# Performance work log

Hardware: AMD Instinct MI355X
Metric: run time of the kernel (lower is better)

Reference implementation:

```python
import jax, jax.numpy as jnp
import numpy as np

NT, NS, NF, NG, NH, ND, HS = 365, 128, 6, 16, 8, 366, 256
EPS = 1e-6


def _divide_p(p, t1, t2):
    # func.divideP: rain/snow partition via arccos temperature interpolation
    r = jnp.clip((t1 + t2) / jnp.maximum(t2 - t1, EPS), -1.0, 1.0)
    vf = jnp.arccos(r) / jnp.pi
    vf = jnp.where(t1 >= 0, 0.0, vf)
    vf = jnp.where(t2 <= 0, 1.0, vf)
    return p * vf, p * (1.0 - vf)  # Ps (snow), Pl (liquid)


def _hard_sigmoid(x):
    return jnp.clip(x / 6.0 + 0.5, 0.0, 1.0)


def setup_inputs():
    key = jax.random.key(0)
    ks = jax.random.split(key, 11)
    prcp = jax.random.uniform(ks[0], (NT, NS)) * 10.0
    evp = jax.random.uniform(ks[1], (NT, NS)) * 5.0
    t1 = jax.random.normal(ks[2], (NT, NS)) * 10.0
    t2 = t1 + jax.random.uniform(ks[3], (NT, NS)) * 10.0 + 0.1
    rad = jax.random.normal(ks[4], (NT, NS))
    hum = jax.random.normal(ks[5], (NT, NS))
    x = jnp.stack([prcp, evp, t1, t2, rad, hum], axis=-1)  # (NT, NS, 6)
    xc = jax.random.normal(ks[6], (NS, NG))

    def lin(k, fan_out, fan_in):
        b = 1.0 / np.sqrt(fan_in)
        kw, kb = jax.random.split(k)
        return (jax.random.uniform(kw, (fan_out, fan_in), minval=-b, maxval=b),
                jax.random.uniform(kb, (fan_out,), minval=-b, maxval=b))

    W_fc, b_fc = lin(ks[7], HS, NG)
    W_g, b_g = lin(ks[8], NH * 6, HS)
    W_kin, b_kin = lin(ks[9], HS, 4)
    W_kout, b_kout = lin(ks[10], NH * 1, HS)
    return dict(x=x, xc=xc, W_fc=W_fc, b_fc=b_fc, W_g=W_g, b_g=b_g,
                W_kin=W_kin, b_kin=b_kin, W_kout=W_kout, b_kout=b_kout)


def reference(x, xc, W_fc, b_fc, W_g, b_g, W_kin, b_kin, W_kout, b_kout):
    prcp, evp, t1, t2 = x[..., 0], x[..., 1], x[..., 2], x[..., 3]
    ps, pl = _divide_p(prcp, t1, t2)  # (NT, NS)
    f = x[..., 2:]  # (NT, NS, 4) time-varying features T1,T2,Rad,Hum

    # getParam (eval mode -> DropMask is identity)
    state = xc @ W_fc.T + b_fc                                   # (NS, HS)
    pk = jnp.tanh(f @ W_kin.T + b_kin + state) @ W_kout.T + b_kout  # (NT, NS, NH)
    pg = jnp.tanh(state) @ W_g.T + b_g                           # (NS, 6*NH)
    km = jnp.exp(pk)                                             # melt rate
    gk = jnp.exp(pg[:, 0:NH]) / 100.0                            # recession
    gl = jnp.exp(pg[:, NH:2 * NH]) * 100.0                       # capacity
    qb = jax.nn.relu(pg[:, 2 * NH:3 * NH]) / 10.0                # baseflow
    ga = jax.nn.softmax(pg[:, 3 * NH:4 * NH], axis=-1)           # bucket areas
    gi = _hard_sigmoid(pg[:, 4 * NH:5 * NH]) / 2.0               # infiltration frac
    ge = jax.nn.relu(pg[:, 5 * NH:6 * NH])                       # evap factor

    sf0 = jnp.zeros((NS, NH), x.dtype)
    d0 = jnp.zeros((NS, NH, ND), x.dtype)

    @jax.checkpoint
    def step(carry, inp):
        sf, d = carry
        ps_t, pl_t, ev_t, km_t = inp
        # snow bucket
        sf1 = sf + ps_t[:, None]
        melt = jnp.minimum(sf1, km_t)
        sf_new = sf1 - melt
        w_in = melt + pl_t[:, None] * gi           # inflow to soil (NS, NH)
        e_pot = ev_t[:, None] * ge
        # StorAge-Selection: age-rank shift, oldest bin pools
        d_sh = jnp.concatenate([w_in[..., None], d[..., :-1]], axis=-1)
        d_sh = d_sh.at[..., -1].add(d[..., -1])
        s = d_sh.sum(-1)
        # evaporation, uniform over ages, capped by storage
        f_ev = jnp.clip(e_pot / jnp.maximum(s, EPS), 0.0, 1.0)
        d1 = d_sh * (1.0 - f_ev[..., None])
        s1 = s * (1.0 - f_ev)
        # surface spill above capacity gl
        q_s = jax.nn.relu(s1 - gl)
        f_s = q_s / jnp.maximum(s1, EPS)
        d2 = d1 * (1.0 - f_s[..., None])
        s2 = s1 - q_s
        # uniform-SAS subsurface discharge
        q_sub = jnp.minimum(s2 * gk + qb, s2)
        f_q = q_sub / jnp.maximum(s2, EPS)
        q_age = d2 * f_q[..., None]                # flux[1]: per-age outflow
        q_age = q_age.at[..., 0].add(q_s)
        d_new = d2 * (1.0 - f_q[..., None])
        q = jnp.sum(q_age.sum(-1) * ga, axis=-1)   # area-weighted discharge (NS,)
        return (sf_new, d_new), q

    (_, _), q_pred = jax.lax.scan(step, (sf0, d0), (ps, pl, evp, km))
    return q_pred  # (NT, NS)
```

## Files before the change

kernel.cpp:

```cpp
#include <hip/hip_runtime.h>
#include <math.h>

#define NT 365
#define NT2 368
#define NS 128
#define NG 16
#define NH 8
#define HS 256
#define NSNH (NS * NH)
#define EPSC 1e-6f

#define WS_PRM 0
#define WS_P   8192

__device__ __forceinline__ float fast_rcp(float v) {
#if __has_builtin(__builtin_amdgcn_rcpf)
    return __builtin_amdgcn_rcpf(v);
#else
    return 1.f / v;
#endif
}
__device__ __forceinline__ float fast_tanh(float xv) {
    float e = __expf(2.f * xv);
    return 1.f - 2.f * fast_rcp(e + 1.f);
}

__global__ __launch_bounds__(256) void k_main(
    const float* __restrict__ x, const float* __restrict__ xc,
    const float* __restrict__ W_fc, const float* __restrict__ b_fc,
    const float* __restrict__ W_g, const float* __restrict__ b_g,
    const float* __restrict__ W_kin, const float* __restrict__ b_kin,
    const float* __restrict__ W_kout, const float* __restrict__ b_kout,
    float* __restrict__ prm, float4* __restrict__ P)
{
    __shared__ float us[HS];
    __shared__ float ts[HS];
    __shared__ __align__(16) float4 wkin_lds[HS];
    __shared__ float wko_lds[8 * 260];
    __shared__ __align__(16) float lds_u[4 * 288];
    __shared__ float pgs[6 * NH];

    int tid = threadIdx.x;
    int wave = tid >> 6, lane = tid & 63;
    int s = blockIdx.x & 127;
    int t0 = (blockIdx.x >> 7) * 4 + wave;
    int h = lane >> 3, jg = lane & 7;

    wkin_lds[tid] = ((const float4*)W_kin)[tid];
#pragma unroll
    for (int i = 0; i < 8; ++i) {
        int idx = tid + 256 * i;
        wko_lds[(idx >> 8) * 260 + (idx & 255)] = W_kout[idx];
    }
    {
        float a = b_fc[tid];
        const float4* wf = (const float4*)(W_fc + tid * NG);
        const float* xr = xc + s * NG;
#pragma unroll
        for (int i = 0; i < 4; ++i) {
            float4 w = wf[i];
            a += xr[4*i] * w.x + xr[4*i+1] * w.y + xr[4*i+2] * w.z + xr[4*i+3] * w.w;
        }
        ts[tid] = tanhf(a);
        us[tid] = a + b_kin[tid];
    }
    __syncthreads();

    float ust[4]; float4 w4[4];
#pragma unroll
    for (int r = 0; r < 4; ++r) {
        ust[r] = us[lane + 64 * r];
        w4[r]  = wkin_lds[lane + 64 * r];
    }
    float4 wwr[8];
#pragma unroll
    for (int k = 0; k < 8; ++k)
        wwr[k] = *(const float4*)(wko_lds + h * 260 + jg * 32 + 4 * k);
    float bko = b_kout[h];

    if (blockIdx.x < NS) {
        for (int k = wave; k < 6 * NH; k += 4) {
            float p = 0.f;
#pragma unroll
            for (int r = 0; r < 4; ++r) {
                int jj = lane + 64 * r;
                p += ts[jj] * W_g[k * HS + jj];
            }
#pragma unroll
            for (int off = 32; off; off >>= 1) p += __shfl_xor(p, off, 64);
            if (lane == 0) pgs[k] = p + b_g[k];
        }
        __syncthreads();
        if (tid < NH) {
            int hh = tid;
            float gk = expf(pgs[hh]) * 0.01f;
            float gl = expf(pgs[NH + hh]) * 100.f;
            float qb = fmaxf(pgs[2 * NH + hh], 0.f) * 0.1f;
            float m = pgs[3 * NH];
#pragma unroll
            for (int i = 1; i < NH; ++i) m = fmaxf(m, pgs[3 * NH + i]);
            float den = 0.f;
#pragma unroll
            for (int i = 0; i < NH; ++i) den += expf(pgs[3 * NH + i] - m);
            float ga = expf(pgs[3 * NH + hh] - m) / den;
            float gi = fminf(fmaxf(pgs[4 * NH + hh] * (1.f / 6.f) + 0.5f, 0.f), 1.f) * 0.5f;
            float ge = fmaxf(pgs[5 * NH + hh], 0.f);
            int o = s * NH + hh;
            prm[0 * NSNH + o] = gk;
            prm[1 * NSNH + o] = gl;
            prm[2 * NSNH + o] = qb;
            prm[3 * NSNH + o] = ga;
            prm[4 * NSNH + o] = gi;
            prm[5 * NSNH + o] = ge;
        }
    }

    float* uw = lds_u + wave * 288;
    int ubase = lane + 4 * (lane >> 5);
    const float4* uuP = (const float4*)(uw + jg * 36);
    int sblk = s >> 3, srem = (s & 7) * 8;

#pragma unroll
    for (int g = 0; g < 8; ++g) {
        int t = t0 + 48 * g;
        if (t >= NT) {
            if (t < NT2 && jg == 0)
                P[(sblk * NT2 + t) * 64 + srem + h] = make_float4(0.f, 0.f, 0.f, 0.f);
            continue;
        }
        const float2* xr2 = (const float2*)(x + (size_t)(t * NS + s) * 6);
        float2 a01 = xr2[0], a23 = xr2[1], a45 = xr2[2];
        float prcp = a01.x, ev = a01.y;
        float f0 = a23.x, f1 = a23.y, f2 = a45.x, f3 = a45.y;
#pragma unroll
        for (int r = 0; r < 4; ++r) {
            float uval = fast_tanh(ust[r] + f0 * w4[r].x + f1 * w4[r].y +
                                   f2 * w4[r].z + f3 * w4[r].w);
            uw[ubase + 72 * r] = uval;
        }
        float r_ = (f0 + f1) / fmaxf(f1 - f0, EPSC);
        r_ = fminf(fmaxf(r_, -1.f), 1.f);
        float vf = acosf(r_) * 0.31830988618379067f;
        if (f0 >= 0.f) vf = 0.f;
        if (f1 <= 0.f) vf = 1.f;
        float psv = prcp * vf;
        float plv = prcp * (1.f - vf);
        float acc = 0.f;
#pragma unroll
        for (int k = 0; k < 8; ++k) {
            float4 a = uuP[k], b = wwr[k];
            acc += a.x * b.x + a.y * b.y + a.z * b.z + a.w * b.w;
        }
        acc += __shfl_xor(acc, 1, 64);
        acc += __shfl_xor(acc, 2, 64);
        acc += __shfl_xor(acc, 4, 64);
        if (jg == 0)
            P[(sblk * NT2 + t) * 64 + srem + h] =
                make_float4(__expf(acc + bko), psv, plv, ev);
    }
}

__global__ __launch_bounds__(64, 1) void k_scan(
    const float4* __restrict__ P, const float* __restrict__ prm,
    float* __restrict__ q)
{
    int lane = threadIdx.x;
    int blk = blockIdx.x;
    int sbase = blk * 8;
    int gofs = blk * 64 + lane;

    float gk = prm[0 * NSNH + gofs];
    float gl = prm[1 * NSNH + gofs];
    float qb = prm[2 * NSNH + gofs];
    float gi = prm[4 * NSNH + gofs];
    float ge = prm[5 * NSNH + gofs];
    float c1 = 1.f - gk, nqb = -qb, nge = -ge;
    int ss0 = lane & 7;
    float gar[8];
#pragma unroll
    for (int hh = 0; hh < 8; ++hh)
        gar[hh] = prm[3 * NSNH + (sbase + ss0) * 8 + hh];

    __shared__ float out_lds[64 * 17];
    float S = 0.f, sf = 0.f;
    const float4* Pb = P + (size_t)blk * (NT2 * 64) + lane;

    float4 A[16], B[16], C[16];

#define LOADC(ci, BUF) { const float4* p_ = Pb + (ci) * 1024; _Pragma("unroll") \
    for (int c = 0; c < 16; ++c) BUF[c] = p_[c * 64]; }

#define WORKC(BUF, tb) { \
    _Pragma("unroll") for (int c = 0; c < 16; ++c) { \
        float4 a = BUF[c]; \
        float sf1 = sf + a.y; \
        float melt = fminf(sf1, a.x); \
        sf = sf1 - melt; \
        float Sw = S + fmaf(a.z, gi, melt); \
        float t2v = fmaf(a.w, nge, Sw); \
        float S1 = fmaxf(t2v, 0.f); \
        float S2 = __builtin_amdgcn_fmed3f(t2v, 0.f, gl); \
        float Sn = fmaxf(fmaf(S2, c1, nqb), 0.f); \
        S = Sn; \
        out_lds[lane * 17 + c] = S1 - Sn; \
    } \
    _Pragma("unroll") for (int it = 0; it < 2; ++it) { \
        int idx = it * 64 + lane; int c = idx >> 3; \
        float sum = 0.f; \
        _Pragma("unroll") for (int hh = 0; hh < 8; ++hh) \
            sum = fmaf(gar[hh], out_lds[(ss0 * 8 + hh) * 17 + c], sum); \
        int t = (tb) + c; \
        if (t < NT) q[t * NS + sbase + ss0] = sum; \
    } }

    LOADC(0, A); LOADC(1, B);
    for (int k = 0; k < 7; ++k) {
        int c3 = 3 * k;
        LOADC(c3 + 2, C); WORKC(A, c3 * 16);
        LOADC(c3 + 3, A); WORKC(B, (c3 + 1) * 16);
        LOADC(c3 + 4, B); WORKC(C, (c3 + 2) * 16);
    }
    WORKC(A, 21 * 16); WORKC(B, 22 * 16);
#undef LOADC
#undef WORKC
}

extern "C" void kernel_launch(void* const* d_in, const int* in_sizes, int n_in,
                              void* d_out, int out_size, void* d_ws, size_t ws_size,
                              hipStream_t stream)
{
    const float* x      = (const float*)d_in[0];
    const float* xc     = (const float*)d_in[1];
    const float* W_fc   = (const float*)d_in[2];
    const float* b_fc   = (const float*)d_in[3];
    const float* W_g    = (const float*)d_in[4];
    const float* b_g    = (const float*)d_in[5];
    const float* W_kin  = (const float*)d_in[6];
    const float* b_kin  = (const float*)d_in[7];
    const float* W_kout = (const float*)d_in[8];
    const float* b_kout = (const float*)d_in[9];
    float* q = (float*)d_out;

    float* ws  = (float*)d_ws;
    float* prm = ws + WS_PRM;
    float4* P  = (float4*)(ws + WS_P);

    hipLaunchKernelGGL(k_main, dim3(1536), dim3(256), 0, stream,
                       x, xc, W_fc, b_fc, W_g, b_g, W_kin, b_kin,
                       W_kout, b_kout, prm, P);

    hipLaunchKernelGGL(k_scan, dim3(16), dim3(64), 0, stream,
                       P, prm, q);
}
```

Baseline: 38.13 us.

## Compute per-timestep kinetic MLP in one thread over hidden dim, shrink grid

Replaces the wave-cooperative layout (lanes split across hidden units, LDS exchange and shuffle reductions) with one thread per timestep looping over all 256 hidden units. It accumulates the 8 outputs in registers using broadcast LDS reads of transposed W_kout. The grid shrinks from 1536 to 256 blocks, and each block covers 184 timesteps for one site. This removes the shuffles and redundant prologue work per block, but gives each thread a long serial loop and leaves fewer threads active, with 72 of 256 idle per block.

```diff
diff --git a/kernel.cpp b/kernel.cpp
--- a/kernel.cpp
+++ b/kernel.cpp
@@ -20,10 +20,14 @@
     return 1.f / v;
 #endif
 }
-__device__ __forceinline__ float fast_tanh(float xv) {
-    float e = __expf(2.f * xv);
-    return 1.f - 2.f * fast_rcp(e + 1.f);
-}
+__device__ __forceinline__ float fexp2(float v) {
+#if __has_builtin(__builtin_amdgcn_exp2f)
+    return __builtin_amdgcn_exp2f(v);
+#else
+    return exp2f(v);
+#endif
+}
+#define TWO_LOG2E 2.8853900817779268f
 
 __global__ __launch_bounds__(256) void k_main(
     const float* __restrict__ x, const float* __restrict__ xc,
@@ -33,24 +37,25 @@
     const float* __restrict__ W_kout, const float* __restrict__ b_kout,
     float* __restrict__ prm, float4* __restrict__ P)
 {
-    __shared__ float us[HS];
+    __shared__ float u0[HS];
     __shared__ float ts[HS];
     __shared__ __align__(16) float4 wkin_lds[HS];
-    __shared__ float wko_lds[8 * 260];
-    __shared__ __align__(16) float lds_u[4 * 288];
+    __shared__ __align__(16) float4 wkoA[HS];
+    __shared__ __align__(16) float4 wkoB[HS];
     __shared__ float pgs[6 * NH];
 
     int tid = threadIdx.x;
-    int wave = tid >> 6, lane = tid & 63;
     int s = blockIdx.x & 127;
-    int t0 = (blockIdx.x >> 7) * 4 + wave;
-    int h = lane >> 3, jg = lane & 7;
+    int th = blockIdx.x >> 7;
 
     wkin_lds[tid] = ((const float4*)W_kin)[tid];
-#pragma unroll
-    for (int i = 0; i < 8; ++i) {
-        int idx = tid + 256 * i;
-        wko_lds[(idx >> 8) * 260 + (idx & 255)] = W_kout[idx];
+    {
+        float4 va, vb;
+        va.x = W_kout[0 * HS + tid]; va.y = W_kout[1 * HS + tid];
+        va.z = W_kout[2 * HS + tid]; va.w = W_kout[3 * HS + tid];
+        vb.x = W_kout[4 * HS + tid]; vb.y = W_kout[5 * HS + tid];
+        vb.z = W_kout[6 * HS + tid]; vb.w = W_kout[7 * HS + tid];
+        wkoA[tid] = va; wkoB[tid] = vb;
     }
     {
         float a = b_fc[tid];
@@ -62,23 +67,12 @@
             a += xr[4*i] * w.x + xr[4*i+1] * w.y + xr[4*i+2] * w.z + xr[4*i+3] * w.w;
         }
         ts[tid] = tanhf(a);
-        us[tid] = a + b_kin[tid];
+        u0[tid] = a + b_kin[tid];
     }
     __syncthreads();
 
-    float ust[4]; float4 w4[4];
-#pragma unroll
-    for (int r = 0; r < 4; ++r) {
-        ust[r] = us[lane + 64 * r];
-        w4[r]  = wkin_lds[lane + 64 * r];
-    }
-    float4 wwr[8];
-#pragma unroll
-    for (int k = 0; k < 8; ++k)
-        wwr[k] = *(const float4*)(wko_lds + h * 260 + jg * 32 + 4 * k);
-    float bko = b_kout[h];
-
     if (blockIdx.x < NS) {
+        int wave = tid >> 6, lane = tid & 63;
         for (int k = wave; k < 6 * NH; k += 4) {
             float p = 0.f;
 #pragma unroll
@@ -115,49 +109,55 @@
         }
     }
 
-    float* uw = lds_u + wave * 288;
-    int ubase = lane + 4 * (lane >> 5);
-    const float4* uuP = (const float4*)(uw + jg * 36);
-    int sblk = s >> 3, srem = (s & 7) * 8;
-
-#pragma unroll
-    for (int g = 0; g < 8; ++g) {
-        int t = t0 + 48 * g;
-        if (t >= NT) {
-            if (t < NT2 && jg == 0)
-                P[(sblk * NT2 + t) * 64 + srem + h] = make_float4(0.f, 0.f, 0.f, 0.f);
-            continue;
-        }
-        const float2* xr2 = (const float2*)(x + (size_t)(t * NS + s) * 6);
-        float2 a01 = xr2[0], a23 = xr2[1], a45 = xr2[2];
-        float prcp = a01.x, ev = a01.y;
-        float f0 = a23.x, f1 = a23.y, f2 = a45.x, f3 = a45.y;
-#pragma unroll
-        for (int r = 0; r < 4; ++r) {
-            float uval = fast_tanh(ust[r] + f0 * w4[r].x + f1 * w4[r].y +
-                                   f2 * w4[r].z + f3 * w4[r].w);
-            uw[ubase + 72 * r] = uval;
-        }
-        float r_ = (f0 + f1) / fmaxf(f1 - f0, EPSC);
-        r_ = fminf(fmaxf(r_, -1.f), 1.f);
-        float vf = acosf(r_) * 0.31830988618379067f;
-        if (f0 >= 0.f) vf = 0.f;
-        if (f1 <= 0.f) vf = 1.f;
-        float psv = prcp * vf;
-        float plv = prcp * (1.f - vf);
-        float acc = 0.f;
-#pragma unroll
-        for (int k = 0; k < 8; ++k) {
-            float4 a = uuP[k], b = wwr[k];
-            acc += a.x * b.x + a.y * b.y + a.z * b.z + a.w * b.w;
-        }
-        acc += __shfl_xor(acc, 1, 64);
-        acc += __shfl_xor(acc, 2, 64);
-        acc += __shfl_xor(acc, 4, 64);
-        if (jg == 0)
-            P[(sblk * NT2 + t) * 64 + srem + h] =
-                make_float4(__expf(acc + bko), psv, plv, ev);
-    }
+    if (tid >= 184) return;
+    int t = th * 184 + tid;
+    float4* Pb = P + ((size_t)(s >> 3) * NT2 + t) * 64 + (s & 7) * 8;
+
+    if (t >= NT) {
+        float4 z = make_float4(0.f, 0.f, 0.f, 0.f);
+#pragma unroll
+        for (int h = 0; h < NH; ++h) Pb[h] = z;
+        return;
+    }
+
+    const float* xr = x + (size_t)(t * NS + s) * 6;
+    float prcp = xr[0], ev = xr[1], f0 = xr[2], f1 = xr[3], f2 = xr[4], f3 = xr[5];
+
+    float a0 = 0.f, a1 = 0.f, a2 = 0.f, a3 = 0.f;
+    float a4 = 0.f, a5 = 0.f, a6 = 0.f, a7 = 0.f;
+#pragma unroll 4
+    for (int j = 0; j < HS; ++j) {
+        float4 w = wkin_lds[j];
+        float arg = u0[j];
+        arg = fmaf(f0, w.x, arg);
+        arg = fmaf(f1, w.y, arg);
+        arg = fmaf(f2, w.z, arg);
+        arg = fmaf(f3, w.w, arg);
+        float e = fexp2(arg * TWO_LOG2E);
+        float tn = 1.f - 2.f * fast_rcp(e + 1.f);
+        float4 wa = wkoA[j], wb = wkoB[j];
+        a0 = fmaf(tn, wa.x, a0); a1 = fmaf(tn, wa.y, a1);
+        a2 = fmaf(tn, wa.z, a2); a3 = fmaf(tn, wa.w, a3);
+        a4 = fmaf(tn, wb.x, a4); a5 = fmaf(tn, wb.y, a5);
+        a6 = fmaf(tn, wb.z, a6); a7 = fmaf(tn, wb.w, a7);
+    }
+
+    float r_ = (f0 + f1) / fmaxf(f1 - f0, EPSC);
+    r_ = fminf(fmaxf(r_, -1.f), 1.f);
+    float vf = acosf(r_) * 0.31830988618379067f;
+    if (f0 >= 0.f) vf = 0.f;
+    if (f1 <= 0.f) vf = 1.f;
+    float psv = prcp * vf;
+    float plv = prcp * (1.f - vf);
+
+    Pb[0] = make_float4(__expf(a0 + b_kout[0]), psv, plv, ev);
+    Pb[1] = make_float4(__expf(a1 + b_kout[1]), psv, plv, ev);
+    Pb[2] = make_float4(__expf(a2 + b_kout[2]), psv, plv, ev);
+    Pb[3] = make_float4(__expf(a3 + b_kout[3]), psv, plv, ev);
+    Pb[4] = make_float4(__expf(a4 + b_kout[4]), psv, plv, ev);
+    Pb[5] = make_float4(__expf(a5 + b_kout[5]), psv, plv, ev);
+    Pb[6] = make_float4(__expf(a6 + b_kout[6]), psv, plv, ev);
+    Pb[7] = make_float4(__expf(a7 + b_kout[7]), psv, plv, ev);
 }
 
 __global__ __launch_bounds__(64, 1) void k_scan(
@@ -245,7 +245,7 @@
     float* prm = ws + WS_PRM;
     float4* P  = (float4*)(ws + WS_P);
 
-    hipLaunchKernelGGL(k_main, dim3(1536), dim3(256), 0, stream,
+    hipLaunchKernelGGL(k_main, dim3(256), dim3(256), 0, stream,
                        x, xc, W_fc, b_fc, W_g, b_g, W_kin, b_kin,
                        W_kout, b_kout, prm, P);
 
```

After: 43.37 us. 1.14x slower.

## Warp-specialize scan: producer waves stage P via LDS ring, consumer reduces outputs

Applied to the files above, without the earlier changes.

The scan kernel becomes four waves. One wave runs the serial recurrence while three waves prefetch input chunks into a triple-buffered LDS ring and do the area-weighted output reduction from a double-buffered LDS output buffer. The main kernel now folds the gi and ge coefficients into a single precomputed inflow term, so the serial chain does fewer FMAs per step. To do that, every k_main block computes the parameter projection, not only the first 128. The change aims to take load latency and reduction work off the serial critical path, at the cost of a block-wide barrier per chunk and redundant parameter work in k_main.

```diff
diff --git a/kernel.cpp b/kernel.cpp
--- a/kernel.cpp
+++ b/kernel.cpp
@@ -9,6 +9,8 @@
 #define HS 256
 #define NSNH (NS * NH)
 #define EPSC 1e-6f
+#define CH 16
+#define NCH 23
 
 #define WS_PRM 0
 #define WS_P   8192
@@ -19,10 +21,6 @@
 #else
     return 1.f / v;
 #endif
-}
-__device__ __forceinline__ float fast_tanh(float xv) {
-    float e = __expf(2.f * xv);
-    return 1.f - 2.f * fast_rcp(e + 1.f);
 }
 
 __global__ __launch_bounds__(256) void k_main(
@@ -39,6 +37,7 @@
     __shared__ float wko_lds[8 * 260];
     __shared__ __align__(16) float lds_u[4 * 288];
     __shared__ float pgs[6 * NH];
+    __shared__ float gie[NH], gee[NH];
 
     int tid = threadIdx.x;
     int wave = tid >> 6, lane = tid & 63;
@@ -78,42 +77,48 @@
         wwr[k] = *(const float4*)(wko_lds + h * 260 + jg * 32 + 4 * k);
     float bko = b_kout[h];
 
-    if (blockIdx.x < NS) {
-        for (int k = wave; k < 6 * NH; k += 4) {
-            float p = 0.f;
-#pragma unroll
-            for (int r = 0; r < 4; ++r) {
-                int jj = lane + 64 * r;
-                p += ts[jj] * W_g[k * HS + jj];
-            }
-#pragma unroll
-            for (int off = 32; off; off >>= 1) p += __shfl_xor(p, off, 64);
-            if (lane == 0) pgs[k] = p + b_g[k];
-        }
-        __syncthreads();
-        if (tid < NH) {
-            int hh = tid;
-            float gk = expf(pgs[hh]) * 0.01f;
-            float gl = expf(pgs[NH + hh]) * 100.f;
-            float qb = fmaxf(pgs[2 * NH + hh], 0.f) * 0.1f;
-            float m = pgs[3 * NH];
-#pragma unroll
-            for (int i = 1; i < NH; ++i) m = fmaxf(m, pgs[3 * NH + i]);
-            float den = 0.f;
-#pragma unroll
-            for (int i = 0; i < NH; ++i) den += expf(pgs[3 * NH + i] - m);
-            float ga = expf(pgs[3 * NH + hh] - m) / den;
-            float gi = fminf(fmaxf(pgs[4 * NH + hh] * (1.f / 6.f) + 0.5f, 0.f), 1.f) * 0.5f;
-            float ge = fmaxf(pgs[5 * NH + hh], 0.f);
-            int o = s * NH + hh;
-            prm[0 * NSNH + o] = gk;
-            prm[1 * NSNH + o] = gl;
-            prm[2 * NSNH + o] = qb;
-            prm[3 * NSNH + o] = ga;
-            prm[4 * NSNH + o] = gi;
-            prm[5 * NSNH + o] = ge;
-        }
-    }
+    for (int k = wave; k < 6 * NH; k += 4) {
+        float p = 0.f;
+#pragma unroll
+        for (int r = 0; r < 4; ++r) {
+            int jj = lane + 64 * r;
+            p += ts[jj] * W_g[k * HS + jj];
+        }
+#pragma unroll
+        for (int off = 32; off; off >>= 1) p += __shfl_xor(p, off, 64);
+        if (lane == 0) pgs[k] = p + b_g[k];
+    }
+    __syncthreads();
+
+    if (tid < NH) {
+        gie[tid] = fminf(fmaxf(pgs[4 * NH + tid] * (1.f / 6.f) + 0.5f, 0.f), 1.f) * 0.5f;
+        gee[tid] = fmaxf(pgs[5 * NH + tid], 0.f);
+    }
+    if (blockIdx.x < NS && tid < NH) {
+        int hh = tid;
+        float gk = expf(pgs[hh]) * 0.01f;
+        float gl = expf(pgs[NH + hh]) * 100.f;
+        float qb = fmaxf(pgs[2 * NH + hh], 0.f) * 0.1f;
+        float m = pgs[3 * NH];
+#pragma unroll
+        for (int i = 1; i < NH; ++i) m = fmaxf(m, pgs[3 * NH + i]);
+        float den = 0.f;
+#pragma unroll
+        for (int i = 0; i < NH; ++i) den += expf(pgs[3 * NH + i] - m);
+        float ga = expf(pgs[3 * NH + hh] - m) / den;
+        float gi = fminf(fmaxf(pgs[4 * NH + hh] * (1.f / 6.f) + 0.5f, 0.f), 1.f) * 0.5f;
+        float ge = fmaxf(pgs[5 * NH + hh], 0.f);
+        int o = s * NH + hh;
+        prm[0 * NSNH + o] = gk;
+        prm[1 * NSNH + o] = gl;
+        prm[2 * NSNH + o] = qb;
+        prm[3 * NSNH + o] = ga;
+        prm[4 * NSNH + o] = gi;
+        prm[5 * NSNH + o] = ge;
+    }
+    __syncthreads();
+
+    float gih = gie[h], geh = gee[h];
 
     float* uw = lds_u + wave * 288;
     int ubase = lane + 4 * (lane >> 5);
@@ -134,9 +139,9 @@
         float f0 = a23.x, f1 = a23.y, f2 = a45.x, f3 = a45.y;
 #pragma unroll
         for (int r = 0; r < 4; ++r) {
-            float uval = fast_tanh(ust[r] + f0 * w4[r].x + f1 * w4[r].y +
-                                   f2 * w4[r].z + f3 * w4[r].w);
-            uw[ubase + 72 * r] = uval;
+            float e = __expf(2.f * (ust[r] + f0 * w4[r].x + f1 * w4[r].y +
+                                    f2 * w4[r].z + f3 * w4[r].w));
+            uw[ubase + 72 * r] = 1.f - 2.f * fast_rcp(e + 1.f);
         }
         float r_ = (f0 + f1) / fmaxf(f1 - f0, EPSC);
         r_ = fminf(fmaxf(r_, -1.f), 1.f);
@@ -156,73 +161,112 @@
         acc += __shfl_xor(acc, 4, 64);
         if (jg == 0)
             P[(sblk * NT2 + t) * 64 + srem + h] =
-                make_float4(__expf(acc + bko), psv, plv, ev);
-    }
-}
-
-__global__ __launch_bounds__(64, 1) void k_scan(
+                make_float4(__expf(acc + bko), psv, plv * gih - ev * geh, 0.f);
+    }
+}
+
+__global__ __launch_bounds__(256, 1) void k_scan(
     const float4* __restrict__ P, const float* __restrict__ prm,
     float* __restrict__ q)
 {
-    int lane = threadIdx.x;
+    __shared__ __align__(16) float4 ring[3][CH][64];
+    __shared__ float outb[2][CH * 72];
+
+    int tid = threadIdx.x, wave = tid >> 6, lane = tid & 63;
     int blk = blockIdx.x;
-    int sbase = blk * 8;
-    int gofs = blk * 64 + lane;
-
-    float gk = prm[0 * NSNH + gofs];
-    float gl = prm[1 * NSNH + gofs];
-    float qb = prm[2 * NSNH + gofs];
-    float gi = prm[4 * NSNH + gofs];
-    float ge = prm[5 * NSNH + gofs];
-    float c1 = 1.f - gk, nqb = -qb, nge = -ge;
-    int ss0 = lane & 7;
+    const float4* Pb = P + (size_t)blk * (NT2 * 64);
+
+    if (wave == 0) {
+        int gofs = blk * 64 + lane;
+        float gk = prm[0 * NSNH + gofs];
+        float gl = prm[1 * NSNH + gofs];
+        float qb = prm[2 * NSNH + gofs];
+        float c1 = 1.f - gk, nqb = -qb;
+        float S = 0.f, sf = 0.f;
+        int obase = (lane >> 3) * 9 + (lane & 7);
+        __syncthreads();
+        for (int c = 0; c < NCH; ++c) {
+            const float4* rs = &ring[c % 3][0][lane];
+            float* ob = &outb[c & 1][obase];
+#pragma unroll
+            for (int st = 0; st < CH; ++st) {
+                float4 a = rs[st * 64];
+                float sf1 = sf + a.y;
+                float melt = fminf(sf1, a.x);
+                sf = sf1 - melt;
+                float t2v = (S + a.z) + melt;
+                float S1 = fmaxf(t2v, 0.f);
+                float S2 = __builtin_amdgcn_fmed3f(t2v, 0.f, gl);
+                float Sn = fmaxf(fmaf(S2, c1, nqb), 0.f);
+                S = Sn;
+                ob[st * 72] = S1 - Sn;
+            }
+            __syncthreads();
+        }
+        return;
+    }
+
+    int w = wave - 1;
+    int nrows = (w == 0) ? 6 : 5;
+    float4 regs[6];
+    int sq = lane & 7;
     float gar[8];
-#pragma unroll
-    for (int hh = 0; hh < 8; ++hh)
-        gar[hh] = prm[3 * NSNH + (sbase + ss0) * 8 + hh];
-
-    __shared__ float out_lds[64 * 17];
-    float S = 0.f, sf = 0.f;
-    const float4* Pb = P + (size_t)blk * (NT2 * 64) + lane;
-
-    float4 A[16], B[16], C[16];
-
-#define LOADC(ci, BUF) { const float4* p_ = Pb + (ci) * 1024; _Pragma("unroll") \
-    for (int c = 0; c < 16; ++c) BUF[c] = p_[c * 64]; }
-
-#define WORKC(BUF, tb) { \
-    _Pragma("unroll") for (int c = 0; c < 16; ++c) { \
-        float4 a = BUF[c]; \
-        float sf1 = sf + a.y; \
-        float melt = fminf(sf1, a.x); \
-        sf = sf1 - melt; \
-        float Sw = S + fmaf(a.z, gi, melt); \
-        float t2v = fmaf(a.w, nge, Sw); \
-        float S1 = fmaxf(t2v, 0.f); \
-        float S2 = __builtin_amdgcn_fmed3f(t2v, 0.f, gl); \
-        float Sn = fmaxf(fmaf(S2, c1, nqb), 0.f); \
-        S = Sn; \
-        out_lds[lane * 17 + c] = S1 - Sn; \
-    } \
-    _Pragma("unroll") for (int it = 0; it < 2; ++it) { \
-        int idx = it * 64 + lane; int c = idx >> 3; \
-        float sum = 0.f; \
-        _Pragma("unroll") for (int hh = 0; hh < 8; ++hh) \
-            sum = fmaf(gar[hh], out_lds[(ss0 * 8 + hh) * 17 + c], sum); \
-        int t = (tb) + c; \
-        if (t < NT) q[t * NS + sbase + ss0] = sum; \
-    } }
-
-    LOADC(0, A); LOADC(1, B);
-    for (int k = 0; k < 7; ++k) {
-        int c3 = 3 * k;
-        LOADC(c3 + 2, C); WORKC(A, c3 * 16);
-        LOADC(c3 + 3, A); WORKC(B, (c3 + 1) * 16);
-        LOADC(c3 + 4, B); WORKC(C, (c3 + 2) * 16);
-    }
-    WORKC(A, 21 * 16); WORKC(B, 22 * 16);
-#undef LOADC
-#undef WORKC
+    if (w >= 1) {
+#pragma unroll
+        for (int hh = 0; hh < 8; ++hh)
+            gar[hh] = prm[3 * NSNH + (blk * 8 + sq) * 8 + hh];
+    }
+#pragma unroll
+    for (int ck = 0; ck < 2; ++ck) {
+        for (int i = 0; i < 6; ++i) {
+            int row = w + 3 * i;
+            if (i < nrows) regs[i] = Pb[(ck * CH + row) * 64 + lane];
+        }
+        for (int i = 0; i < 6; ++i) {
+            int row = w + 3 * i;
+            if (i < nrows) ring[ck][row][lane] = regs[i];
+        }
+    }
+    for (int i = 0; i < 6; ++i) {
+        int row = w + 3 * i;
+        if (i < nrows) regs[i] = Pb[(2 * CH + row) * 64 + lane];
+    }
+    __syncthreads();
+
+    for (int c = 0; c < NCH; ++c) {
+        if (c + 2 < NCH) {
+            int slot = (c + 2) % 3;
+            for (int i = 0; i < 6; ++i) {
+                int row = w + 3 * i;
+                if (i < nrows) ring[slot][row][lane] = regs[i];
+            }
+            if (c + 3 < NCH) {
+                for (int i = 0; i < 6; ++i) {
+                    int row = w + 3 * i;
+                    if (i < nrows) regs[i] = Pb[((c + 3) * CH + row) * 64 + lane];
+                }
+            }
+        }
+        if (w >= 1 && c >= 1) {
+            int cq = (w - 1) * 8 + (lane >> 3);
+            const float* ob = &outb[(c - 1) & 1][cq * 72 + sq * 9];
+            float sum = 0.f;
+#pragma unroll
+            for (int hh = 0; hh < 8; ++hh) sum = fmaf(gar[hh], ob[hh], sum);
+            int t = (c - 1) * CH + cq;
+            if (t < NT) q[t * NS + blk * 8 + sq] = sum;
+        }
+        __syncthreads();
+    }
+    if (w >= 1) {
+        int cq = (w - 1) * 8 + (lane >> 3);
+        const float* ob = &outb[(NCH - 1) & 1][cq * 72 + sq * 9];
+        float sum = 0.f;
+#pragma unroll
+        for (int hh = 0; hh < 8; ++hh) sum = fmaf(gar[hh], ob[hh], sum);
+        int t = (NCH - 1) * CH + cq;
+        if (t < NT) q[t * NS + blk * 8 + sq] = sum;
+    }
 }
 
 extern "C" void kernel_launch(void* const* d_in, const int* in_sizes, int n_in,
@@ -249,6 +293,6 @@
                        x, xc, W_fc, b_fc, W_g, b_g, W_kin, b_kin,
                        W_kout, b_kout, prm, P);
 
-    hipLaunchKernelGGL(k_scan, dim3(16), dim3(64), 0, stream,
+    hipLaunchKernelGGL(k_scan, dim3(16), dim3(256), 0, stream,
                        P, prm, q);
 }
```

Result: slower. 66.19 us (+73.6%).
